# Kernel tuning notes

Hardware: AMD Instinct MI355X
Metric: run time of the kernel (lower is better)

Reference implementation:

```python
import jax, jax.numpy as jnp
import numpy as np

N = 100000   # nodes
E = 600000   # edges
C = 128      # feature dim
LN_EPS = 1e-5


def setup_inputs() -> dict:
    key = jax.random.key(0)
    k = jax.random.split(key, 5)
    h = jax.random.normal(k[0], (N, C), dtype=jnp.float32)
    edge_index = jax.random.randint(k[1], (2, E), 0, N)
    edge_weight = jax.random.uniform(k[2], (E,), dtype=jnp.float32)
    W = jax.random.normal(k[3], (C, C), dtype=jnp.float32) / np.sqrt(C).astype(np.float32)
    b = jax.random.normal(k[4], (C,), dtype=jnp.float32) * 0.01
    gamma = jnp.ones((C,), jnp.float32)
    beta = jnp.zeros((C,), jnp.float32)
    return {"h": h, "edge_index": edge_index, "edge_weight": edge_weight,
            "W": W, "b": b, "gamma": gamma, "beta": beta}


def reference(h, edge_index, edge_weight, W, b, gamma, beta):
    n = h.shape[0]
    self_idx = jnp.arange(n)
    # add self-loops with weight 1
    src = jnp.concatenate([edge_index[0], self_idx])
    dst = jnp.concatenate([edge_index[1], self_idx])
    ew = jnp.concatenate([edge_weight, jnp.ones((n,), h.dtype)])
    # symmetric normalization: deg over dst, d = deg^{-1/2} clamped at 1e4
    deg = jax.ops.segment_sum(ew, dst, num_segments=n)
    d = jnp.minimum(deg ** -0.5, 10000.0)
    norm = d[src] * ew * d[dst]                      # [E+N]
    msg = h[src] * norm[:, None]                     # [E+N, C]
    agg = jax.ops.segment_sum(msg, dst, num_segments=n)  # [N, C]
    # linear + residual + layernorm + exact GELU (dropout = identity in eval)
    x = agg @ W.T + b + h
    mean = jnp.mean(x, axis=-1, keepdims=True)
    var = jnp.mean(jnp.square(x - mean), axis=-1, keepdims=True)
    y = gamma * (x - mean) * jax.lax.rsqrt(var + LN_EPS) + beta
    return jax.nn.gelu(y, approximate=False)
```

## Files before the change

### kernel.cpp

```cpp
#include <hip/hip_runtime.h>

constexpr int C = 128;
#define SCAN_CHUNK 1024

typedef __attribute__((ext_vector_type(8))) short short8;
typedef __attribute__((ext_vector_type(4))) float f32x4;
typedef __attribute__((ext_vector_type(2))) unsigned int u32x2;

__device__ __forceinline__ unsigned short f2bf(float f) {
  unsigned int u = __float_as_uint(f);
  unsigned int r = (u + 0x7fffu + ((u >> 16) & 1u)) >> 16;
  return (unsigned short)r;
}
__device__ __forceinline__ float bfl(unsigned int p) { return __uint_as_float(p << 16); }
__device__ __forceinline__ float bfh(unsigned int p) { return __uint_as_float(p & 0xffff0000u); }

template <int DO_HB>
__global__ void k_prep_all(const float* __restrict__ W, unsigned short* __restrict__ Wb,
                           const float* __restrict__ h, unsigned short* __restrict__ hb,
                           int total4, unsigned long long* __restrict__ packed, int n) {
  const int stride = gridDim.x * blockDim.x;
  const int gid = blockIdx.x * blockDim.x + threadIdx.x;
  for (int i = gid; i < C * C / 4; i += stride) {
    float4 w = ((const float4*)W)[i];
    uint2 pk;
    pk.x = f2bf(w.x) | ((unsigned int)f2bf(w.y) << 16);
    pk.y = f2bf(w.z) | ((unsigned int)f2bf(w.w) << 16);
    ((uint2*)Wb)[i] = pk;
  }
  if (DO_HB) {
    for (int i = gid; i < total4; i += stride) {
      f32x4 w = __builtin_nontemporal_load(&((const f32x4*)h)[i]);
      u32x2 pk;
      pk.x = f2bf(w.x) | ((unsigned int)f2bf(w.y) << 16);
      pk.y = f2bf(w.z) | ((unsigned int)f2bf(w.w) << 16);
      ((u32x2*)hb)[i] = pk;
    }
  }
  for (int i = gid; i < n; i += stride) packed[i] = 0ull;
}

__global__ void k_edge_deg(const int* __restrict__ dst, const float* __restrict__ ew,
                           unsigned long long* __restrict__ packed,
                           int* __restrict__ slot, int e) {
  int i = blockIdx.x * blockDim.x + threadIdx.x;
  if (i < e) {
    unsigned long long enc =
        (1ull << 40) | (unsigned long long)(ew[i] * 4294967296.0f);
    unsigned long long old = atomicAdd(&packed[dst[i]], enc);
    slot[i] = (int)(old >> 40);
  }
}

__global__ void k_scan1(const unsigned long long* __restrict__ packed,
                        float* __restrict__ d, int* __restrict__ excl,
                        int* __restrict__ sums, int n) {
  __shared__ int l[256];
  const int t = threadIdx.x;
  const int base = blockIdx.x * SCAN_CHUNK + t * 4;
  int v0 = 0, v1 = 0, v2 = 0, v3 = 0;
  const float fs = 1.0f / 4294967296.0f;
  const unsigned long long M = (1ull << 40) - 1ull;
  if (base + 0 < n) { unsigned long long p = packed[base + 0]; v0 = (int)(p >> 40);
    d[base + 0] = fminf(1.0f / sqrtf(1.0f + (float)(p & M) * fs), 10000.0f); }
  if (base + 1 < n) { unsigned long long p = packed[base + 1]; v1 = (int)(p >> 40);
    d[base + 1] = fminf(1.0f / sqrtf(1.0f + (float)(p & M) * fs), 10000.0f); }
  if (base + 2 < n) { unsigned long long p = packed[base + 2]; v2 = (int)(p >> 40);
    d[base + 2] = fminf(1.0f / sqrtf(1.0f + (float)(p & M) * fs), 10000.0f); }
  if (base + 3 < n) { unsigned long long p = packed[base + 3]; v3 = (int)(p >> 40);
    d[base + 3] = fminf(1.0f / sqrtf(1.0f + (float)(p & M) * fs), 10000.0f); }
  const int s = v0 + v1 + v2 + v3;
  l[t] = s; __syncthreads();
  for (int off = 1; off < 256; off <<= 1) {
    int x = 0;
    if (t >= off) x = l[t - off];
    __syncthreads();
    l[t] += x;
    __syncthreads();
  }
  int ex = l[t] - s;
  if (t == 255) sums[blockIdx.x] = l[t];
  if (base + 0 < n) excl[base + 0] = ex;  ex += v0;
  if (base + 1 < n) excl[base + 1] = ex;  ex += v1;
  if (base + 2 < n) excl[base + 2] = ex;  ex += v2;
  if (base + 3 < n) excl[base + 3] = ex;
}

__global__ void k_scan23(int* __restrict__ rowptr, const int* __restrict__ sums,
                         int nb, int n, int e) {
  __shared__ int l[256];
  __shared__ int pre[256];
  const int t = threadIdx.x;
  const int s = (t < nb) ? sums[t] : 0;
  l[t] = s; __syncthreads();
  for (int off = 1; off < 256; off <<= 1) {
    int x = 0;
    if (t >= off) x = l[t - off];
    __syncthreads();
    l[t] += x;
    __syncthreads();
  }
  pre[t] = l[t] - s;
  __syncthreads();
  const int i = blockIdx.x * 256 + t;
  if (i < n) rowptr[i] += pre[i >> 10];
  else if (i == n) rowptr[n] = e;
}

__global__ void k_scatter(const int* __restrict__ src, const int* __restrict__ dst,
                          const float* __restrict__ ew, const float* __restrict__ d,
                          const int* __restrict__ rowptr, const int* __restrict__ slot,
                          int2* __restrict__ meta, int e) {
  int i = blockIdx.x * blockDim.x + threadIdx.x;
  if (i < e) {
    int t = dst[i], s = src[i];
    float nm = d[s] * ew[i] * d[t];
    int p = rowptr[t] + slot[i];
    meta[p] = make_int2(s, __float_as_int(nm));
  }
}

template <int USE_HB, int OUT_BF>
__global__ void k_gather(const int* __restrict__ rowptr, const int2* __restrict__ meta,
                         const float* __restrict__ d, const float* __restrict__ h,
                         const unsigned short* __restrict__ hb,
                         float* __restrict__ aggf, unsigned short* __restrict__ aggb,
                         int n) {
  int g = blockIdx.x * blockDim.x + threadIdx.x;
  int v = g >> 5, lane = g & 31;
  if (v >= n) return;
  const int cb = lane * 4;
  const float dv = d[v];
  const float dd = dv * dv;
  const u32x2* mp = (const u32x2*)meta;
  float4 acc;
  if (USE_HB) {
    uint2 hv = *(const uint2*)(hb + (size_t)v * C + cb);
    acc = make_float4(bfl(hv.x) * dd, bfh(hv.x) * dd, bfl(hv.y) * dd, bfh(hv.y) * dd);
  } else {
    float4 hv = *(const float4*)(h + (size_t)v * C + cb);
    acc = make_float4(hv.x * dd, hv.y * dd, hv.z * dd, hv.w * dd);
  }
  int p = rowptr[v];
  const int end = rowptr[v + 1];
  if (USE_HB) {
    for (; p + 4 <= end; p += 4) {
      u32x2 m0 = __builtin_nontemporal_load(mp + p);
      u32x2 m1 = __builtin_nontemporal_load(mp + p + 1);
      u32x2 m2 = __builtin_nontemporal_load(mp + p + 2);
      u32x2 m3 = __builtin_nontemporal_load(mp + p + 3);
      float n0 = __uint_as_float(m0.y), n1 = __uint_as_float(m1.y);
      float n2 = __uint_as_float(m2.y), n3 = __uint_as_float(m3.y);
      uint2 x0 = *(const uint2*)(hb + (size_t)m0.x * C + cb);
      uint2 x1 = *(const uint2*)(hb + (size_t)m1.x * C + cb);
      uint2 x2 = *(const uint2*)(hb + (size_t)m2.x * C + cb);
      uint2 x3 = *(const uint2*)(hb + (size_t)m3.x * C + cb);
      acc.x += bfl(x0.x) * n0 + bfl(x1.x) * n1 + bfl(x2.x) * n2 + bfl(x3.x) * n3;
      acc.y += bfh(x0.x) * n0 + bfh(x1.x) * n1 + bfh(x2.x) * n2 + bfh(x3.x) * n3;
      acc.z += bfl(x0.y) * n0 + bfl(x1.y) * n1 + bfl(x2.y) * n2 + bfl(x3.y) * n3;
      acc.w += bfh(x0.y) * n0 + bfh(x1.y) * n1 + bfh(x2.y) * n2 + bfh(x3.y) * n3;
    }
    for (; p < end; ++p) {
      u32x2 m0 = __builtin_nontemporal_load(mp + p);
      float n0 = __uint_as_float(m0.y);
      uint2 x0 = *(const uint2*)(hb + (size_t)m0.x * C + cb);
      acc.x += bfl(x0.x) * n0; acc.y += bfh(x0.x) * n0;
      acc.z += bfl(x0.y) * n0; acc.w += bfh(x0.y) * n0;
    }
  } else {
    for (; p + 4 <= end; p += 4) {
      u32x2 m0 = __builtin_nontemporal_load(mp + p);
      u32x2 m1 = __builtin_nontemporal_load(mp + p + 1);
      u32x2 m2 = __builtin_nontemporal_load(mp + p + 2);
      u32x2 m3 = __builtin_nontemporal_load(mp + p + 3);
      float n0 = __uint_as_float(m0.y), n1 = __uint_as_float(m1.y);
      float n2 = __uint_as_float(m2.y), n3 = __uint_as_float(m3.y);
      float4 x0 = *(const float4*)(h + (size_t)m0.x * C + cb);
      float4 x1 = *(const float4*)(h + (size_t)m1.x * C + cb);
      float4 x2 = *(const float4*)(h + (size_t)m2.x * C + cb);
      float4 x3 = *(const float4*)(h + (size_t)m3.x * C + cb);
      acc.x += x0.x * n0 + x1.x * n1 + x2.x * n2 + x3.x * n3;
      acc.y += x0.y * n0 + x1.y * n1 + x2.y * n2 + x3.y * n3;
      acc.z += x0.z * n0 + x1.z * n1 + x2.z * n2 + x3.z * n3;
      acc.w += x0.w * n0 + x1.w * n1 + x2.w * n2 + x3.w * n3;
    }
    for (; p < end; ++p) {
      u32x2 m0 = __builtin_nontemporal_load(mp + p);
      float n0 = __uint_as_float(m0.y);
      float4 x0 = *(const float4*)(h + (size_t)m0.x * C + cb);
      acc.x += x0.x * n0; acc.y += x0.y * n0; acc.z += x0.z * n0; acc.w += x0.w * n0;
    }
  }
  if (OUT_BF) {
    uint2 pk;
    pk.x = f2bf(acc.x) | ((unsigned int)f2bf(acc.y) << 16);
    pk.y = f2bf(acc.z) | ((unsigned int)f2bf(acc.w) << 16);
    *(uint2*)(aggb + (size_t)v * C + cb) = pk;
  } else {
    *(float4*)(aggf + (size_t)v * C + cb) = acc;
  }
}

#define TM 64

template <int IN_BF, int RES_BF>
__launch_bounds__(256, 3)
__global__ void k_mfma_ln_gelu(const float* __restrict__ aggf,
                               const unsigned short* __restrict__ aggb,
                               const float* __restrict__ h,
                               const unsigned short* __restrict__ hb,
                               const unsigned short* __restrict__ Wb,
                               const float* __restrict__ b,
                               const float* __restrict__ gamma, const float* __restrict__ beta,
                               float* __restrict__ out, int n) {
  __shared__ char lds[48 * 1024];
  char* Wl = lds;
  char* Al = lds + 32768;
  const int tid = threadIdx.x;
  const int row0 = blockIdx.x * TM;

  #pragma unroll
  for (int i = 0; i < 8; ++i) {
    int u = tid + i * 256;
    int j = u >> 4, un = u & 15;
    uint4 w = ((const uint4*)Wb)[u];
    *(uint4*)(Wl + j * 256 + ((un * 16) ^ ((j & 7) << 4))) = w;
  }
  #pragma unroll
  for (int i = 0; i < 8; ++i) {
    int u = tid + i * 256;
    int j = u >> 5;
    int rr = row0 + j; if (rr >= n) rr = n - 1;
    uint2 pk;
    if (IN_BF) {
      pk = ((const uint2*)(aggb + (size_t)rr * C))[u & 31];
    } else {
      float4 a = ((const float4*)(aggf + (size_t)rr * C))[u & 31];
      pk.x = f2bf(a.x) | ((unsigned int)f2bf(a.y) << 16);
      pk.y = f2bf(a.z) | ((unsigned int)f2bf(a.w) << 16);
    }
    *(uint2*)(Al + j * 256 + (((u & 31) * 8) ^ ((j & 7) << 4))) = pk;
  }
  __syncthreads();

  const int lane = tid & 63;
  const int wt   = tid >> 6;
  const int c16  = lane & 15;
  const int quad = lane >> 4;

  f32x4 acc[8];
  #pragma unroll
  for (int jt = 0; jt < 8; ++jt) acc[jt] = (f32x4){0.f, 0.f, 0.f, 0.f};

  const int abase = (wt * 16 + c16) * 256;
  const int swz   = (c16 & 7) << 4;
  #pragma unroll
  for (int ks = 0; ks < 4; ++ks) {
    const int koff = ks * 64 + quad * 16;
    short8 af_agg = *(const short8*)(Al + abase + (koff ^ swz));
    #pragma unroll
    for (int jt = 0; jt < 8; ++jt) {
      short8 af_w = *(const short8*)(Wl + (jt * 16 + c16) * 256 + (koff ^ swz));
      acc[jt] = __builtin_amdgcn_mfma_f32_16x16x32_bf16(af_w, af_agg, acc[jt], 0, 0, 0);
    }
  }

  const int node = row0 + wt * 16 + c16;
  const bool ok = node < n;
  const int jb = quad * 4;
  float s = 0.f, t2 = 0.f;
  #pragma unroll
  for (int jt = 0; jt < 8; ++jt) {
    const int j = jt * 16 + jb;
    float4 b4 = *(const float4*)(b + j);
    float r0 = 0.f, r1 = 0.f, r2 = 0.f, r3 = 0.f;
    if (ok) {
      if (RES_BF) {
        uint2 rh = *(const uint2*)(hb + (size_t)node * C + j);
        r0 = bfl(rh.x); r1 = bfh(rh.x); r2 = bfl(rh.y); r3 = bfh(rh.y);
      } else {
        float4 rh = *(const float4*)(h + (size_t)node * C + j);
        r0 = rh.x; r1 = rh.y; r2 = rh.z; r3 = rh.w;
      }
    }
    acc[jt][0] += b4.x + r0;
    acc[jt][1] += b4.y + r1;
    acc[jt][2] += b4.z + r2;
    acc[jt][3] += b4.w + r3;
    #pragma unroll
    for (int i = 0; i < 4; ++i) { float v = acc[jt][i]; s += v; t2 += v * v; }
  }
  s  += __shfl_xor(s, 16);  t2 += __shfl_xor(t2, 16);
  s  += __shfl_xor(s, 32);  t2 += __shfl_xor(t2, 32);
  const float inv = 1.0f / C;
  const float mean = s * inv;
  const float var  = t2 * inv - mean * mean;
  const float rstd = rsqrtf(var + 1e-5f);
  if (ok) {
    float* orow = out + (size_t)node * C;
    #pragma unroll
    for (int jt = 0; jt < 8; ++jt) {
      const int j = jt * 16 + jb;
      float4 g4  = *(const float4*)(gamma + j);
      float4 be4 = *(const float4*)(beta + j);
      float4 o;
      float y;
      y = g4.x * ((acc[jt][0] - mean) * rstd) + be4.x; o.x = 0.5f * y * (1.0f + erff(y * 0.70710678118f));
      y = g4.y * ((acc[jt][1] - mean) * rstd) + be4.y; o.y = 0.5f * y * (1.0f + erff(y * 0.70710678118f));
      y = g4.z * ((acc[jt][2] - mean) * rstd) + be4.z; o.z = 0.5f * y * (1.0f + erff(y * 0.70710678118f));
      y = g4.w * ((acc[jt][3] - mean) * rstd) + be4.w; o.w = 0.5f * y * (1.0f + erff(y * 0.70710678118f));
      *(float4*)(orow + j) = o;
    }
  }
}

extern "C" void kernel_launch(void* const* d_in, const int* in_sizes, int n_in,
                              void* d_out, int out_size, void* d_ws, size_t ws_size,
                              hipStream_t stream) {
  const float* h     = (const float*)d_in[0];
  const int*   ei    = (const int*)d_in[1];
  const float* ew    = (const float*)d_in[2];
  const float* W     = (const float*)d_in[3];
  const float* b     = (const float*)d_in[4];
  const float* gamma = (const float*)d_in[5];
  const float* beta  = (const float*)d_in[6];

  const int n = in_sizes[0] / C;
  const int e = in_sizes[2];
  const int* src = ei;
  const int* dst = ei + e;

  float* out = (float*)d_out;

  int2* meta    = (int2*)d_ws;
  unsigned long long* packed = (unsigned long long*)(meta + e);
  int* slot     = (int*)(packed + n);
  float* d      = (float*)(slot + e);
  int* rowptr   = (int*)(d + n);
  int* sums     = rowptr + (n + 1);
  unsigned short* Wb = (unsigned short*)(sums + 256);
  unsigned short* hb = Wb + C * C;
  unsigned short* aggb = hb + (size_t)n * C;

  const size_t need_mid  = (size_t)((char*)(hb + (size_t)n * C) - (char*)d_ws);
  const size_t need_full = (size_t)((char*)(aggb + (size_t)n * C) - (char*)d_ws);
  const int mode = (ws_size >= need_full) ? 2 : (ws_size >= need_mid) ? 1 : 0;

  const int nb = (n + SCAN_CHUNK - 1) / SCAN_CHUNK;
  const int total4 = n * C / 4;

  if (mode >= 1)
    k_prep_all<1><<<1024, 256, 0, stream>>>(W, Wb, h, hb, total4, packed, n);
  else
    k_prep_all<0><<<1024, 256, 0, stream>>>(W, Wb, h, hb, total4, packed, n);

  k_edge_deg<<<(e + 255) / 256, 256, 0, stream>>>(dst, ew, packed, slot, e);
  k_scan1   <<<nb, 256, 0, stream>>>(packed, d, rowptr, sums, n);
  k_scan23  <<<(n + 256) / 256, 256, 0, stream>>>(rowptr, sums, nb, n, e);
  k_scatter <<<(e + 255) / 256, 256, 0, stream>>>(src, dst, ew, d, rowptr, slot, meta, e);

  const long gthreads = (long)n * 32;
  const int ggrid = (int)((gthreads + 255) / 256);
  const int mgrid = (n + TM - 1) / TM;

  if (mode == 2) {
    k_gather<1, 1><<<ggrid, 256, 0, stream>>>(rowptr, meta, d, h, hb, out, aggb, n);
    k_mfma_ln_gelu<1, 1><<<mgrid, 256, 0, stream>>>(out, aggb, h, hb, Wb, b, gamma, beta, out, n);
  } else if (mode == 1) {
    k_gather<1, 0><<<ggrid, 256, 0, stream>>>(rowptr, meta, d, h, hb, out, aggb, n);
    k_mfma_ln_gelu<0, 1><<<mgrid, 256, 0, stream>>>(out, aggb, h, hb, Wb, b, gamma, beta, out, n);
  } else {
    k_gather<0, 0><<<ggrid, 256, 0, stream>>>(rowptr, meta, d, h, hb, out, aggb, n);
    k_mfma_ln_gelu<0, 0><<<mgrid, 256, 0, stream>>>(out, aggb, h, hb, Wb, b, gamma, beta, out, n);
  }
}
```

Baseline: 147.1 us.

## Fuse edge degree into prep kernel and fold scan finalisation into last block

Merges the per-edge degree/slot atomics into the W/h bf16 conversion kernel, replacing the in-kernel zeroing of the packed counters with an async memset. The second scan launch is removed: the last block of scan1, detected via an atomic counter, scans the per-block sums into a small prefix table. Consumers now compute row offsets as excl[v] + pre[v>>10] instead of reading a finished rowptr. This cuts two kernel launches and their serialization gaps, at the cost of an extra memset, threadfences, and a second indexed load in scatter and gather.

```diff
diff --git a/kernel.cpp b/kernel.cpp
--- a/kernel.cpp
+++ b/kernel.cpp
@@ -16,11 +16,20 @@
 __device__ __forceinline__ float bfh(unsigned int p) { return __uint_as_float(p & 0xffff0000u); }
 
 template <int DO_HB>
-__global__ void k_prep_all(const float* __restrict__ W, unsigned short* __restrict__ Wb,
-                           const float* __restrict__ h, unsigned short* __restrict__ hb,
-                           int total4, unsigned long long* __restrict__ packed, int n) {
+__global__ void k_prep_edge(const float* __restrict__ W, unsigned short* __restrict__ Wb,
+                            const float* __restrict__ h, unsigned short* __restrict__ hb,
+                            int total4,
+                            const int* __restrict__ dst, const float* __restrict__ ew,
+                            unsigned long long* __restrict__ packed,
+                            int* __restrict__ slot, int e) {
   const int stride = gridDim.x * blockDim.x;
   const int gid = blockIdx.x * blockDim.x + threadIdx.x;
+  for (int i = gid; i < e; i += stride) {
+    unsigned long long enc =
+        (1ull << 40) | (unsigned long long)(ew[i] * 4294967296.0f);
+    unsigned long long old = atomicAdd(&packed[dst[i]], enc);
+    slot[i] = (int)(old >> 40);
+  }
   for (int i = gid; i < C * C / 4; i += stride) {
     float4 w = ((const float4*)W)[i];
     uint2 pk;
@@ -37,25 +46,14 @@
       ((u32x2*)hb)[i] = pk;
     }
   }
-  for (int i = gid; i < n; i += stride) packed[i] = 0ull;
-}
-
-__global__ void k_edge_deg(const int* __restrict__ dst, const float* __restrict__ ew,
-                           unsigned long long* __restrict__ packed,
-                           int* __restrict__ slot, int e) {
-  int i = blockIdx.x * blockDim.x + threadIdx.x;
-  if (i < e) {
-    unsigned long long enc =
-        (1ull << 40) | (unsigned long long)(ew[i] * 4294967296.0f);
-    unsigned long long old = atomicAdd(&packed[dst[i]], enc);
-    slot[i] = (int)(old >> 40);
-  }
 }
 
 __global__ void k_scan1(const unsigned long long* __restrict__ packed,
                         float* __restrict__ d, int* __restrict__ excl,
-                        int* __restrict__ sums, int n) {
+                        int* __restrict__ sums, int* __restrict__ pre,
+                        int* __restrict__ counter, int n, int nb) {
   __shared__ int l[256];
+  __shared__ int lastFlag;
   const int t = threadIdx.x;
   const int base = blockIdx.x * SCAN_CHUNK + t * 4;
   int v0 = 0, v1 = 0, v2 = 0, v3 = 0;
@@ -79,53 +77,52 @@
     __syncthreads();
   }
   int ex = l[t] - s;
-  if (t == 255) sums[blockIdx.x] = l[t];
   if (base + 0 < n) excl[base + 0] = ex;  ex += v0;
   if (base + 1 < n) excl[base + 1] = ex;  ex += v1;
   if (base + 2 < n) excl[base + 2] = ex;  ex += v2;
   if (base + 3 < n) excl[base + 3] = ex;
-}
-
-__global__ void k_scan23(int* __restrict__ rowptr, const int* __restrict__ sums,
-                         int nb, int n, int e) {
-  __shared__ int l[256];
-  __shared__ int pre[256];
-  const int t = threadIdx.x;
-  const int s = (t < nb) ? sums[t] : 0;
-  l[t] = s; __syncthreads();
-  for (int off = 1; off < 256; off <<= 1) {
-    int x = 0;
-    if (t >= off) x = l[t - off];
-    __syncthreads();
-    l[t] += x;
-    __syncthreads();
-  }
-  pre[t] = l[t] - s;
+
+  if (t == 255) atomicExch(&sums[blockIdx.x], l[255]);
+  __threadfence();
   __syncthreads();
-  const int i = blockIdx.x * 256 + t;
-  if (i < n) rowptr[i] += pre[i >> 10];
-  else if (i == n) rowptr[n] = e;
+  if (t == 0) lastFlag = (atomicAdd(counter, 1) == nb - 1);
+  __syncthreads();
+  if (lastFlag) {
+    __threadfence();
+    const int sv = (t < nb) ? atomicAdd(&sums[t], 0) : 0;
+    l[t] = sv; __syncthreads();
+    for (int off = 1; off < 256; off <<= 1) {
+      int x = 0;
+      if (t >= off) x = l[t - off];
+      __syncthreads();
+      l[t] += x;
+      __syncthreads();
+    }
+    pre[t] = l[t] - sv;
+  }
 }
 
 __global__ void k_scatter(const int* __restrict__ src, const int* __restrict__ dst,
                           const float* __restrict__ ew, const float* __restrict__ d,
-                          const int* __restrict__ rowptr, const int* __restrict__ slot,
+                          const int* __restrict__ excl, const int* __restrict__ pre,
+                          const int* __restrict__ slot,
                           int2* __restrict__ meta, int e) {
   int i = blockIdx.x * blockDim.x + threadIdx.x;
   if (i < e) {
     int t = dst[i], s = src[i];
     float nm = d[s] * ew[i] * d[t];
-    int p = rowptr[t] + slot[i];
+    int p = excl[t] + pre[t >> 10] + slot[i];
     meta[p] = make_int2(s, __float_as_int(nm));
   }
 }
 
 template <int USE_HB, int OUT_BF>
-__global__ void k_gather(const int* __restrict__ rowptr, const int2* __restrict__ meta,
+__global__ void k_gather(const int* __restrict__ excl, const int* __restrict__ pre,
+                         const int2* __restrict__ meta,
                          const float* __restrict__ d, const float* __restrict__ h,
                          const unsigned short* __restrict__ hb,
                          float* __restrict__ aggf, unsigned short* __restrict__ aggb,
-                         int n) {
+                         int n, int e) {
   int g = blockIdx.x * blockDim.x + threadIdx.x;
   int v = g >> 5, lane = g & 31;
   if (v >= n) return;
@@ -141,8 +138,8 @@
     float4 hv = *(const float4*)(h + (size_t)v * C + cb);
     acc = make_float4(hv.x * dd, hv.y * dd, hv.z * dd, hv.w * dd);
   }
-  int p = rowptr[v];
-  const int end = rowptr[v + 1];
+  int p = excl[v] + pre[v >> 10];
+  const int end = (v + 1 < n) ? (excl[v + 1] + pre[(v + 1) >> 10]) : e;
   if (USE_HB) {
     for (; p + 4 <= end; p += 4) {
       u32x2 m0 = __builtin_nontemporal_load(mp + p);
@@ -334,11 +331,13 @@
 
   int2* meta    = (int2*)d_ws;
   unsigned long long* packed = (unsigned long long*)(meta + e);
-  int* slot     = (int*)(packed + n);
+  int* counter  = (int*)(packed + n);
+  int* slot     = counter + 2;
   float* d      = (float*)(slot + e);
-  int* rowptr   = (int*)(d + n);
-  int* sums     = rowptr + (n + 1);
-  unsigned short* Wb = (unsigned short*)(sums + 256);
+  int* excl     = (int*)(d + n);
+  int* sums     = excl + n;
+  int* pre      = sums + 256;
+  unsigned short* Wb = (unsigned short*)(pre + 256);
   unsigned short* hb = Wb + C * C;
   unsigned short* aggb = hb + (size_t)n * C;
 
@@ -349,28 +348,28 @@
   const int nb = (n + SCAN_CHUNK - 1) / SCAN_CHUNK;
   const int total4 = n * C / 4;
 
+  hipMemsetAsync(packed, 0, (size_t)n * 8 + 8, stream);
+
   if (mode >= 1)
-    k_prep_all<1><<<1024, 256, 0, stream>>>(W, Wb, h, hb, total4, packed, n);
+    k_prep_edge<1><<<2048, 256, 0, stream>>>(W, Wb, h, hb, total4, dst, ew, packed, slot, e);
   else
-    k_prep_all<0><<<1024, 256, 0, stream>>>(W, Wb, h, hb, total4, packed, n);
-
-  k_edge_deg<<<(e + 255) / 256, 256, 0, stream>>>(dst, ew, packed, slot, e);
-  k_scan1   <<<nb, 256, 0, stream>>>(packed, d, rowptr, sums, n);
-  k_scan23  <<<(n + 256) / 256, 256, 0, stream>>>(rowptr, sums, nb, n, e);
-  k_scatter <<<(e + 255) / 256, 256, 0, stream>>>(src, dst, ew, d, rowptr, slot, meta, e);
+    k_prep_edge<0><<<2048, 256, 0, stream>>>(W, Wb, h, hb, total4, dst, ew, packed, slot, e);
+
+  k_scan1  <<<nb, 256, 0, stream>>>(packed, d, excl, sums, pre, counter, n, nb);
+  k_scatter<<<(e + 255) / 256, 256, 0, stream>>>(src, dst, ew, d, excl, pre, slot, meta, e);
 
   const long gthreads = (long)n * 32;
   const int ggrid = (int)((gthreads + 255) / 256);
   const int mgrid = (n + TM - 1) / TM;
 
   if (mode == 2) {
-    k_gather<1, 1><<<ggrid, 256, 0, stream>>>(rowptr, meta, d, h, hb, out, aggb, n);
+    k_gather<1, 1><<<ggrid, 256, 0, stream>>>(excl, pre, meta, d, h, hb, out, aggb, n, e);
     k_mfma_ln_gelu<1, 1><<<mgrid, 256, 0, stream>>>(out, aggb, h, hb, Wb, b, gamma, beta, out, n);
   } else if (mode == 1) {
-    k_gather<1, 0><<<ggrid, 256, 0, stream>>>(rowptr, meta, d, h, hb, out, aggb, n);
+    k_gather<1, 0><<<ggrid, 256, 0, stream>>>(excl, pre, meta, d, h, hb, out, aggb, n, e);
     k_mfma_ln_gelu<0, 1><<<mgrid, 256, 0, stream>>>(out, aggb, h, hb, Wb, b, gamma, beta, out, n);
   } else {
-    k_gather<0, 0><<<ggrid, 256, 0, stream>>>(rowptr, meta, d, h, hb, out, aggb, n);
+    k_gather<0, 0><<<ggrid, 256, 0, stream>>>(excl, pre, meta, d, h, hb, out, aggb, n, e);
     k_mfma_ln_gelu<0, 0><<<mgrid, 256, 0, stream>>>(out, aggb, h, hb, Wb, b, gamma, beta, out, n);
   }
 }
```

Result: slower. 161.4 us (+9.8%).
